# Kernel optimization log

Measured on AMD Instinct MI355X. Metric: run time of the kernel, lower is better.

## Reference

```python
import jax, jax.numpy as jnp
import numpy as np

N_NODES = 50000
N_EDGES = 300000
F_IN = 11
D = 256


def _gcn_conv(h, src, dst, deg_inv_sqrt, W, b, n):
    """PyG GCNConv: out = D^{-1/2} (A + I) D^{-1/2} (h W) + b.
    src/dst already include self-loops; deg_inv_sqrt precomputed."""
    norm = deg_inv_sqrt[src] * deg_inv_sqrt[dst]          # [E+N]
    hw = h @ W                                            # [N, D]
    msg = hw[src] * norm[:, None]                         # [E+N, D]
    out = jax.ops.segment_sum(msg, dst, num_segments=n)   # [N, D]
    return out + b


def setup_inputs() -> dict:
    key = jax.random.key(0)
    ks = jax.random.split(key, 8)
    x = jax.random.normal(ks[0], (N_NODES, F_IN), dtype=jnp.float32)
    edge_index = jax.random.randint(ks[1], (2, N_EDGES), 0, N_NODES, dtype=jnp.int32)
    s = 0.05
    W_embed = jax.random.normal(ks[2], (F_IN, D), dtype=jnp.float32) * s
    b_embed = jnp.zeros((D,), dtype=jnp.float32)
    W1 = jax.random.normal(ks[3], (D, D), dtype=jnp.float32) * s
    b1 = jnp.zeros((D,), dtype=jnp.float32)
    W2 = jax.random.normal(ks[4], (D, D), dtype=jnp.float32) * s
    b2 = jnp.zeros((D,), dtype=jnp.float32)
    return {"x": x, "edge_index": edge_index, "W_embed": W_embed, "b_embed": b_embed,
            "W1": W1, "b1": b1, "W2": W2, "b2": b2}


def reference(x, edge_index, W_embed, b_embed, W1, b1, W2, b2):
    n = x.shape[0]
    # add self-loops (PyG GCNConv default add_self_loops=True)
    loop = jnp.arange(n, dtype=edge_index.dtype)
    src = jnp.concatenate([edge_index[0], loop])
    dst = jnp.concatenate([edge_index[1], loop])
    # symmetric normalization: deg over target index with unit edge weights
    deg = jax.ops.segment_sum(jnp.ones(src.shape, dtype=x.dtype), dst, num_segments=n)
    deg_inv_sqrt = jnp.where(deg > 0, jax.lax.rsqrt(jnp.maximum(deg, 1e-12)), 0.0)

    h = jax.nn.relu(x @ W_embed + b_embed)                # embed + relu
    h = jax.nn.relu(_gcn_conv(h, src, dst, deg_inv_sqrt, W1, b1, n))
    h = _gcn_conv(h, src, dst, deg_inv_sqrt, W2, b2, n)
    return h
```

## Files before the change

### kernel.cpp

```cpp
#include <hip/hip_runtime.h>

#define N_NODES 50000
#define N_EDGES 300000
#define N_TOT   350000
#define D       256
#define MPAD    50048

typedef __attribute__((ext_vector_type(8))) short bf16x8;
typedef __attribute__((ext_vector_type(4))) float f32x4;
typedef __attribute__((ext_vector_type(8))) unsigned short u16x8;

__device__ __forceinline__ float bf2f(unsigned short b) {
    union { unsigned u; float f; } v; v.u = ((unsigned)b) << 16; return v.f;
}
__device__ __forceinline__ unsigned short f2bf(float f) {
    union { float f; unsigned u; } v; v.f = f;
    unsigned u = v.u;
    unsigned r = (u + 0x7FFFu + ((u >> 16) & 1u)) >> 16;
    return (unsigned short)r;
}

__global__ void hist_kernel(const int* __restrict__ ei, int* __restrict__ cnt) {
    int e = blockIdx.x * 256 + threadIdx.x;
    if (e >= N_TOT) return;
    int dst = (e < N_EDGES) ? ei[N_EDGES + e] : (e - N_EDGES);
    atomicAdd(&cnt[dst], 1);
}

__global__ void dis_kernel(const int* __restrict__ cnt, float* __restrict__ dis) {
    int i = blockIdx.x * 256 + threadIdx.x;
    if (i >= N_NODES) return;
    dis[i] = rsqrtf((float)cnt[i]);
}

__global__ void scan_kernel(const int* __restrict__ cnt, int* __restrict__ rowptr) {
    __shared__ int wsum[16];
    __shared__ int chunk_total;
    int t = threadIdx.x;
    int lane = t & 63, wid = t >> 6;
    int carry = 0;
    if (t == 0) rowptr[0] = 0;
    for (int base = 0; base < N_NODES; base += 4096) {
        int i = base + t * 4;
        int4 v = {0, 0, 0, 0};
        if (i < N_NODES) v = *(const int4*)(cnt + i);
        int s0 = v.x, s1 = s0 + v.y, s2 = s1 + v.z, s3 = s2 + v.w;
        int s = s3;
        #pragma unroll
        for (int d = 1; d < 64; d <<= 1) {
            int u = __shfl_up(s, d, 64);
            if (lane >= d) s += u;
        }
        if (lane == 63) wsum[wid] = s;
        __syncthreads();
        if (t == 0) {
            int acc = 0;
            #pragma unroll
            for (int k = 0; k < 16; ++k) { int tmp = wsum[k]; wsum[k] = acc; acc += tmp; }
            chunk_total = acc;
        }
        __syncthreads();
        int excl = (s - s3) + wsum[wid] + carry;
        if (i < N_NODES) {
            rowptr[i + 1] = excl + s0;
            rowptr[i + 2] = excl + s1;
            rowptr[i + 3] = excl + s2;
            rowptr[i + 4] = excl + s3;
        }
        carry += chunk_total;
        __syncthreads();
    }
}

__global__ void fill_kernel(const int* __restrict__ ei, const int* __restrict__ rowptr,
                            int* __restrict__ fc, const float* __restrict__ dis,
                            int* __restrict__ esrc, float* __restrict__ enorm) {
    int e = blockIdx.x * 256 + threadIdx.x;
    if (e >= N_TOT) return;
    int src, dst;
    if (e < N_EDGES) { src = ei[e]; dst = ei[N_EDGES + e]; }
    else             { src = dst = e - N_EDGES; }
    int pos = rowptr[dst] + atomicAdd(&fc[dst], 1);
    esrc[pos]  = src;
    enorm[pos] = dis[src] * dis[dst];
}

__global__ void transpose_kernel(const float* __restrict__ W1,
                                 const float* __restrict__ W2,
                                 unsigned short* __restrict__ Wt1,
                                 unsigned short* __restrict__ Wt2) {
    int b = blockIdx.x, t = threadIdx.x;
    if (b < D) Wt1[b * D + t] = f2bf(W1[t * D + b]);
    else       Wt2[(b - D) * D + t] = f2bf(W2[t * D + (b - D)]);
}

__global__ void embed_kernel(const float* __restrict__ x,
                             const float* __restrict__ We,
                             const float* __restrict__ be,
                             unsigned short* __restrict__ hA) {
    int t = threadIdx.x;
    float w[11];
    #pragma unroll
    for (int k = 0; k < 11; ++k) w[k] = We[k * D + t];
    float b = be[t];
    int node0 = blockIdx.x * 8;
    #pragma unroll
    for (int ni = 0; ni < 8; ++ni) {
        int node = node0 + ni;
        float acc = 0.f;
        if (node < N_NODES) {
            acc = b;
            #pragma unroll
            for (int k = 0; k < 11; ++k) acc += x[node * 11 + k] * w[k];
            acc = fmaxf(acc, 0.f);
        }
        hA[(size_t)node * D + t] = f2bf(acc);
    }
}

__global__ __launch_bounds__(256) void gemm_kernel(const unsigned short* __restrict__ A,
                                                   const unsigned short* __restrict__ Bt,
                                                   unsigned short* __restrict__ C) {
    int wid  = threadIdx.x >> 6;
    int lane = threadIdx.x & 63;
    int m0 = blockIdx.x * 64;
    int n0 = wid * 64;
    int q = lane >> 4, r = lane & 15;

    f32x4 acc[4][4] = {};
    const unsigned short* Ap = A  + (size_t)(m0 + r) * D + q * 8;
    const unsigned short* Bp = Bt + (size_t)(n0 + r) * D + q * 8;

    for (int kk = 0; kk < D; kk += 32) {
        bf16x8 a[4], b[4];
        #pragma unroll
        for (int mt = 0; mt < 4; ++mt)
            a[mt] = *(const bf16x8*)(Ap + (size_t)mt * 16 * D + kk);
        #pragma unroll
        for (int nt = 0; nt < 4; ++nt)
            b[nt] = *(const bf16x8*)(Bp + (size_t)nt * 16 * D + kk);
        #pragma unroll
        for (int mt = 0; mt < 4; ++mt)
            #pragma unroll
            for (int nt = 0; nt < 4; ++nt)
                acc[mt][nt] = __builtin_amdgcn_mfma_f32_16x16x32_bf16(a[mt], b[nt], acc[mt][nt], 0, 0, 0);
    }
    #pragma unroll
    for (int mt = 0; mt < 4; ++mt)
        #pragma unroll
        for (int nt = 0; nt < 4; ++nt) {
            int col  = n0 + nt * 16 + r;
            int rowb = m0 + mt * 16 + q * 4;
            #pragma unroll
            for (int i = 0; i < 4; ++i)
                C[(size_t)(rowb + i) * D + col] = f2bf(acc[mt][nt][i]);
        }
}

__global__ __launch_bounds__(256) void agg_kernel(const unsigned short* __restrict__ hw,
                                                  const int* __restrict__ rowptr,
                                                  const int* __restrict__ esrc,
                                                  const float* __restrict__ enorm,
                                                  const float* __restrict__ bias,
                                                  unsigned short* __restrict__ out_bf,
                                                  float* __restrict__ out_f32,
                                                  int mode) {
    int wid  = threadIdx.x >> 6;
    int lane = threadIdx.x & 63;
    int node = blockIdx.x * 4 + wid;
    if (node >= N_NODES) return;
    int s0 = rowptr[node], s1 = rowptr[node + 1];
    int half = lane >> 5, hl = lane & 31;

    float acc[8] = {};
    for (int base = s0; base < s1; base += 64) {
        int ec = s1 - base; if (ec > 64) ec = 64;
        int   srcl = 0; float nml = 0.f;
        if (lane < ec) { srcl = esrc[base + lane]; nml = enorm[base + lane]; }
        int it = (ec + 1) >> 1;
        for (int i = 0; i < it; ++i) {
            int   e  = 2 * i + half;
            int   s  = __shfl(srcl, e, 64);
            float nm = __shfl(nml, e, 64);
            u16x8 hv = *(const u16x8*)(hw + (size_t)s * D + hl * 8);
            #pragma unroll
            for (int k = 0; k < 8; ++k) acc[k] += nm * bf2f(hv[k]);
        }
    }
    #pragma unroll
    for (int k = 0; k < 8; ++k) acc[k] += __shfl_xor(acc[k], 32, 64);

    if (lane < 32) {
        int c = hl * 8;
        float4 bv0 = *(const float4*)(bias + c);
        float4 bv1 = *(const float4*)(bias + c + 4);
        acc[0] += bv0.x; acc[1] += bv0.y; acc[2] += bv0.z; acc[3] += bv0.w;
        acc[4] += bv1.x; acc[5] += bv1.y; acc[6] += bv1.z; acc[7] += bv1.w;
        if (mode) {
            u16x8 ov;
            #pragma unroll
            for (int k = 0; k < 8; ++k) ov[k] = f2bf(fmaxf(acc[k], 0.f));
            *(u16x8*)(out_bf + (size_t)node * D + c) = ov;
        } else {
            float4 o0 = { acc[0], acc[1], acc[2], acc[3] };
            float4 o1 = { acc[4], acc[5], acc[6], acc[7] };
            *(float4*)(out_f32 + (size_t)node * D + c)     = o0;
            *(float4*)(out_f32 + (size_t)node * D + c + 4) = o1;
        }
    }
}

extern "C" void kernel_launch(void* const* d_in, const int* in_sizes, int n_in,
                              void* d_out, int out_size, void* d_ws, size_t ws_size,
                              hipStream_t stream) {
    const float* x  = (const float*)d_in[0];
    const int*   ei = (const int*)d_in[1];
    const float* We = (const float*)d_in[2];
    const float* be = (const float*)d_in[3];
    const float* W1 = (const float*)d_in[4];
    const float* b1 = (const float*)d_in[5];
    const float* W2 = (const float*)d_in[6];
    const float* b2 = (const float*)d_in[7];
    float* out = (float*)d_out;

    char* w = (char*)d_ws;
    auto alloc = [&](size_t bytes) {
        char* p = w;
        w += (bytes + 255) & ~(size_t)255;
        return p;
    };
    int*            cnt    = (int*)alloc((size_t)N_NODES * 4);
    int*            rowptr = (int*)alloc((size_t)(N_NODES + 1) * 4);
    float*          dis    = (float*)alloc((size_t)N_NODES * 4);
    int*            esrc   = (int*)alloc((size_t)N_TOT * 4);
    float*          enorm  = (float*)alloc((size_t)N_TOT * 4);
    unsigned short* Wt1    = (unsigned short*)alloc((size_t)D * D * 2);
    unsigned short* Wt2    = (unsigned short*)alloc((size_t)D * D * 2);
    unsigned short* hA     = (unsigned short*)alloc((size_t)MPAD * D * 2);
    unsigned short* hW     = (unsigned short*)alloc((size_t)MPAD * D * 2);

    hipMemsetAsync(cnt, 0, (size_t)N_NODES * 4, stream);
    hist_kernel<<<(N_TOT + 255) / 256, 256, 0, stream>>>(ei, cnt);
    dis_kernel<<<(N_NODES + 255) / 256, 256, 0, stream>>>(cnt, dis);
    scan_kernel<<<1, 1024, 0, stream>>>(cnt, rowptr);
    hipMemsetAsync(cnt, 0, (size_t)N_NODES * 4, stream);
    fill_kernel<<<(N_TOT + 255) / 256, 256, 0, stream>>>(ei, rowptr, cnt, dis, esrc, enorm);
    transpose_kernel<<<2 * D, 256, 0, stream>>>(W1, W2, Wt1, Wt2);

    embed_kernel<<<MPAD / 8, 256, 0, stream>>>(x, We, be, hA);

    gemm_kernel<<<MPAD / 64, 256, 0, stream>>>(hA, Wt1, hW);
    agg_kernel<<<(N_NODES + 3) / 4, 256, 0, stream>>>(hW, rowptr, esrc, enorm, b1, hA, nullptr, 1);

    gemm_kernel<<<MPAD / 64, 256, 0, stream>>>(hA, Wt2, hW);
    agg_kernel<<<(N_NODES + 3) / 4, 256, 0, stream>>>(hW, rowptr, esrc, enorm, b2, nullptr, out, 0);
}
```

Measured before the change: 283.0 us.

## Stage GEMM tiles through LDS and parallelize the row-pointer scan

```diff
diff --git a/kernel.cpp b/kernel.cpp
--- a/kernel.cpp
+++ b/kernel.cpp
@@ -5,6 +5,7 @@
 #define N_TOT   350000
 #define D       256
 #define MPAD    50048
+#define SCAN_B  196
 
 typedef __attribute__((ext_vector_type(8))) short bf16x8;
 typedef __attribute__((ext_vector_type(4))) float f32x4;
@@ -19,6 +20,11 @@
     unsigned r = (u + 0x7FFFu + ((u >> 16) & 1u)) >> 16;
     return (unsigned short)r;
 }
+__device__ __forceinline__ void g2lds16(const unsigned short* g, unsigned short* l) {
+    __builtin_amdgcn_global_load_lds(
+        (const __attribute__((address_space(1))) void*)g,
+        (__attribute__((address_space(3))) void*)l, 16, 0, 0);
+}
 
 __global__ void hist_kernel(const int* __restrict__ ei, int* __restrict__ cnt) {
     int e = blockIdx.x * 256 + threadIdx.x;
@@ -33,43 +39,50 @@
     dis[i] = rsqrtf((float)cnt[i]);
 }
 
-__global__ void scan_kernel(const int* __restrict__ cnt, int* __restrict__ rowptr) {
-    __shared__ int wsum[16];
-    __shared__ int chunk_total;
-    int t = threadIdx.x;
-    int lane = t & 63, wid = t >> 6;
-    int carry = 0;
-    if (t == 0) rowptr[0] = 0;
-    for (int base = 0; base < N_NODES; base += 4096) {
-        int i = base + t * 4;
-        int4 v = {0, 0, 0, 0};
-        if (i < N_NODES) v = *(const int4*)(cnt + i);
-        int s0 = v.x, s1 = s0 + v.y, s2 = s1 + v.z, s3 = s2 + v.w;
-        int s = s3;
-        #pragma unroll
-        for (int d = 1; d < 64; d <<= 1) {
-            int u = __shfl_up(s, d, 64);
-            if (lane >= d) s += u;
-        }
-        if (lane == 63) wsum[wid] = s;
-        __syncthreads();
-        if (t == 0) {
-            int acc = 0;
-            #pragma unroll
-            for (int k = 0; k < 16; ++k) { int tmp = wsum[k]; wsum[k] = acc; acc += tmp; }
-            chunk_total = acc;
-        }
-        __syncthreads();
-        int excl = (s - s3) + wsum[wid] + carry;
-        if (i < N_NODES) {
-            rowptr[i + 1] = excl + s0;
-            rowptr[i + 2] = excl + s1;
-            rowptr[i + 3] = excl + s2;
-            rowptr[i + 4] = excl + s3;
-        }
-        carry += chunk_total;
-        __syncthreads();
-    }
+__global__ void scan1_kernel(const int* __restrict__ cnt, int* __restrict__ locs,
+                             int* __restrict__ bsum) {
+    __shared__ int ws[4];
+    int t = threadIdx.x, lane = t & 63, wv = t >> 6;
+    int i = blockIdx.x * 256 + t;
+    int v = (i < N_NODES) ? cnt[i] : 0;
+    int s = v;
+    #pragma unroll
+    for (int d = 1; d < 64; d <<= 1) {
+        int u = __shfl_up(s, d, 64);
+        if (lane >= d) s += u;
+    }
+    if (lane == 63) ws[wv] = s;
+    __syncthreads();
+    int off = 0;
+    #pragma unroll
+    for (int k = 0; k < 4; ++k) if (k < wv) off += ws[k];
+    s += off;
+    if (i < N_NODES) locs[i] = s;
+    if (t == 255) bsum[blockIdx.x] = s;
+}
+__global__ void scan2_kernel(int* __restrict__ bsum) {
+    __shared__ int ws[4];
+    int t = threadIdx.x, lane = t & 63, wv = t >> 6;
+    int v = (t < SCAN_B) ? bsum[t] : 0;
+    int s = v;
+    #pragma unroll
+    for (int d = 1; d < 64; d <<= 1) {
+        int u = __shfl_up(s, d, 64);
+        if (lane >= d) s += u;
+    }
+    if (lane == 63) ws[wv] = s;
+    __syncthreads();
+    int off = 0;
+    #pragma unroll
+    for (int k = 0; k < 4; ++k) if (k < wv) off += ws[k];
+    s += off;
+    if (t < SCAN_B) bsum[t] = s - v;
+}
+__global__ void scan3_kernel(const int* __restrict__ locs, const int* __restrict__ bsum,
+                             int* __restrict__ rowptr) {
+    int i = blockIdx.x * 256 + threadIdx.x;
+    if (i == 0) rowptr[0] = 0;
+    if (i < N_NODES) rowptr[i + 1] = locs[i] + bsum[i >> 8];
 }
 
 __global__ void fill_kernel(const int* __restrict__ ei, const int* __restrict__ rowptr,
@@ -121,24 +134,42 @@
 __global__ __launch_bounds__(256) void gemm_kernel(const unsigned short* __restrict__ A,
                                                    const unsigned short* __restrict__ Bt,
                                                    unsigned short* __restrict__ C) {
-    int wid  = threadIdx.x >> 6;
-    int lane = threadIdx.x & 63;
-    int m0 = blockIdx.x * 64;
-    int n0 = wid * 64;
+    __shared__ unsigned short lA[128 * 32];
+    __shared__ unsigned short lB[128 * 32];
+    int t = threadIdx.x;
+    int wv = t >> 6, lane = t & 63;
+    int m0 = blockIdx.x * 128;
+    int n0 = blockIdx.y * 128;
+    int moff = (wv & 1) * 64, noff = (wv >> 1) * 64;
     int q = lane >> 4, r = lane & 15;
 
+    int srow = t >> 2;
+    int skof = (t & 3) * 8;
+
+    const unsigned short* Ag0 = A  + (size_t)(m0 + srow) * D + skof;
+    const unsigned short* Ag1 = Ag0 + (size_t)64 * D;
+    const unsigned short* Bg0 = Bt + (size_t)(n0 + srow) * D + skof;
+    const unsigned short* Bg1 = Bg0 + (size_t)64 * D;
+    unsigned short* lA0 = lA + t * 8;
+    unsigned short* lA1 = lA0 + 64 * 32;
+    unsigned short* lB0 = lB + t * 8;
+    unsigned short* lB1 = lB0 + 64 * 32;
+
     f32x4 acc[4][4] = {};
-    const unsigned short* Ap = A  + (size_t)(m0 + r) * D + q * 8;
-    const unsigned short* Bp = Bt + (size_t)(n0 + r) * D + q * 8;
-
     for (int kk = 0; kk < D; kk += 32) {
+        __syncthreads();
+        g2lds16(Ag0 + kk, lA0);
+        g2lds16(Ag1 + kk, lA1);
+        g2lds16(Bg0 + kk, lB0);
+        g2lds16(Bg1 + kk, lB1);
+        __syncthreads();
         bf16x8 a[4], b[4];
         #pragma unroll
         for (int mt = 0; mt < 4; ++mt)
-            a[mt] = *(const bf16x8*)(Ap + (size_t)mt * 16 * D + kk);
+            a[mt] = *(const bf16x8*)(lA + (moff + mt * 16 + r) * 32 + q * 8);
         #pragma unroll
         for (int nt = 0; nt < 4; ++nt)
-            b[nt] = *(const bf16x8*)(Bp + (size_t)nt * 16 * D + kk);
+            b[nt] = *(const bf16x8*)(lB + (noff + nt * 16 + r) * 32 + q * 8);
         #pragma unroll
         for (int mt = 0; mt < 4; ++mt)
             #pragma unroll
@@ -149,8 +180,8 @@
     for (int mt = 0; mt < 4; ++mt)
         #pragma unroll
         for (int nt = 0; nt < 4; ++nt) {
-            int col  = n0 + nt * 16 + r;
-            int rowb = m0 + mt * 16 + q * 4;
+            int col  = n0 + noff + nt * 16 + r;
+            int rowb = m0 + moff + mt * 16 + q * 4;
             #pragma unroll
             for (int i = 0; i < 4; ++i)
                 C[(size_t)(rowb + i) * D + col] = f2bf(acc[mt][nt][i]);
@@ -231,6 +262,8 @@
     };
     int*            cnt    = (int*)alloc((size_t)N_NODES * 4);
     int*            rowptr = (int*)alloc((size_t)(N_NODES + 1) * 4);
+    int*            locs   = (int*)alloc((size_t)N_NODES * 4);
+    int*            bsum   = (int*)alloc((size_t)SCAN_B * 4);
     float*          dis    = (float*)alloc((size_t)N_NODES * 4);
     int*            esrc   = (int*)alloc((size_t)N_TOT * 4);
     float*          enorm  = (float*)alloc((size_t)N_TOT * 4);
@@ -242,16 +275,19 @@
     hipMemsetAsync(cnt, 0, (size_t)N_NODES * 4, stream);
     hist_kernel<<<(N_TOT + 255) / 256, 256, 0, stream>>>(ei, cnt);
     dis_kernel<<<(N_NODES + 255) / 256, 256, 0, stream>>>(cnt, dis);
-    scan_kernel<<<1, 1024, 0, stream>>>(cnt, rowptr);
+    scan1_kernel<<<SCAN_B, 256, 0, stream>>>(cnt, locs, bsum);
+    scan2_kernel<<<1, 256, 0, stream>>>(bsum);
+    scan3_kernel<<<SCAN_B, 256, 0, stream>>>(locs, bsum, rowptr);
     hipMemsetAsync(cnt, 0, (size_t)N_NODES * 4, stream);
     fill_kernel<<<(N_TOT + 255) / 256, 256, 0, stream>>>(ei, rowptr, cnt, dis, esrc, enorm);
     transpose_kernel<<<2 * D, 256, 0, stream>>>(W1, W2, Wt1, Wt2);
 
     embed_kernel<<<MPAD / 8, 256, 0, stream>>>(x, We, be, hA);
 
-    gemm_kernel<<<MPAD / 64, 256, 0, stream>>>(hA, Wt1, hW);
+    dim3 ggrid(MPAD / 128, 2);
+    gemm_kernel<<<ggrid, 256, 0, stream>>>(hA, Wt1, hW);
     agg_kernel<<<(N_NODES + 3) / 4, 256, 0, stream>>>(hW, rowptr, esrc, enorm, b1, hA, nullptr, 1);
 
-    gemm_kernel<<<MPAD / 64, 256, 0, stream>>>(hA, Wt2, hW);
+    gemm_kernel<<<ggrid, 256, 0, stream>>>(hA, Wt2, hW);
     agg_kernel<<<(N_NODES + 3) / 4, 256, 0, stream>>>(hW, rowptr, esrc, enorm, b2, nullptr, out, 0);
 }
```

New measurement: 242.0 us. 1.17x faster.
